# Optimization experiments

Hardware: AMD Instinct MI355X
Metric: run time of the kernel (lower is better)

Reference implementation:

```python
import jax, jax.numpy as jnp
import numpy as np

B, D, O = 512, 256, 128  # batch, input_dim, output_dim


def setup_inputs() -> dict:
    key = jax.random.key(0)
    k1, k2, k3, k4, k5, k6 = jax.random.split(key, 6)
    eyeD = jnp.eye(D, dtype=jnp.float32)
    # density-like inputs: diagonal offset keeps the trace denominator well-conditioned
    x_real = jax.random.normal(k1, (B, D, D), dtype=jnp.float32) + 2.0 * eyeD
    x_imag = jax.random.normal(k2, (B, D, D), dtype=jnp.float32)
    # weight = identity + small perturbation (module inits to [eye, zeros] stacked)
    w_r = eyeD + 0.02 * jax.random.normal(k3, (D, D), dtype=jnp.float32)
    w_i = 0.02 * jax.random.normal(k4, (D, D), dtype=jnp.float32)
    weight = jnp.stack([w_r, w_i], axis=-1)  # [D, D, 2]
    rand_w = jax.random.uniform(k5, (O,), dtype=jnp.float32)
    lam = jax.random.uniform(k6, (1,), dtype=jnp.float32)
    return {"x_real": x_real, "x_imag": x_imag, "weight": weight,
            "rand_w": rand_w, "lam": lam}


def reference(x_real, x_imag, weight, rand_w, lam):
    out_dim = rand_w.shape[0]
    U_r = weight[:, :, 0]  # [D, D]
    U_i = weight[:, :, 1]
    # evolution: (U_r + i U_i) X (U_r + i U_i)^H, batched over b
    R = jnp.einsum('ij,bjk->bik', U_r, x_real) - jnp.einsum('ij,bjk->bik', U_i, x_imag)
    I = jnp.einsum('ij,bjk->bik', U_i, x_real) + jnp.einsum('ij,bjk->bik', U_r, x_imag)
    out_r = jnp.einsum('bik,jk->bij', R, U_r) + jnp.einsum('bik,jk->bij', I, U_i)
    out_i = jnp.einsum('bik,jk->bij', I, U_r) - jnp.einsum('bik,jk->bij', R, U_i)
    # input_dim >= output_dim branch: top-left block, normalized by trace of real part
    sub_r = out_r[:, :out_dim, :out_dim]
    sub_i = out_i[:, :out_dim, :out_dim]
    tr = jnp.trace(sub_r, axis1=1, axis2=2)[:, None, None]  # [B,1,1]
    norm_r = sub_r / tr
    norm_i = sub_i / tr
    p = jax.nn.softmax(rand_w, axis=-1)
    s = jax.nn.sigmoid(lam[0])
    output_r = s * norm_r + (1.0 - s) * jnp.diag(p)
    output_i = s * norm_i
    return (output_r, output_i)
```

## Files before the change

kernel.cpp:

```cpp
#include <hip/hip_runtime.h>
#include <hip/hip_bf16.h>


typedef __attribute__((ext_vector_type(4))) float f32x4;
typedef __attribute__((ext_vector_type(8))) short bf16x8;

static __device__ __forceinline__ short f2bf(float f) {
    unsigned u = __float_as_uint(f);
    u += 0x7fffu + ((u >> 16) & 1u);
    return (short)(u >> 16);
}

static __device__ __forceinline__ unsigned cvtpk2(float lo, float hi) {
    union { __hip_bfloat162 h; unsigned u; } c;
    c.h = __float22bfloat162_rn(float2{lo, hi});
    return c.u;
}

static __device__ __forceinline__ uint2 cvt2(f32x4 v) {
    uint2 r;
    r.x = cvtpk2(v[0], v[1]);
    r.y = cvtpk2(v[2], v[3]);
    return r;
}

static __device__ __forceinline__ f32x4 mfma16(bf16x8 a, bf16x8 b, f32x4 c) {
    return __builtin_amdgcn_mfma_f32_16x16x32_bf16(a, b, c, 0, 0, 0);
}

__global__ void qprep_u(const float* __restrict__ wt,
                        short* __restrict__ Ur,  short* __restrict__ Ui,
                        short* __restrict__ Upr, short* __restrict__ Upi) {
    int idx = blockIdx.x * 256 + threadIdx.x;
    int j = idx >> 8, k = idx & 255;
    float2 v = ((const float2*)wt)[idx];
    short br = f2bf(v.x), bi = f2bf(v.y);
    Ur[idx] = br;
    Ui[idx] = bi;
    int g = j >> 4, s = k >> 5;
    int lanep = (j & 15) | (((k >> 3) & 3) << 4);
    int p = ((g * 8 + s) * 64 + lanep) * 8 + (k & 7);
    Upr[p] = br;
    Upi[p] = bi;
}

__global__ void qprep_ps(const float* __restrict__ rw, const float* __restrict__ lm,
                         float* __restrict__ pv, float* __restrict__ sv) {
    int t = threadIdx.x;
    float w0 = rw[t], w1 = rw[t + 64];
    float m = fmaxf(w0, w1);
    #pragma unroll
    for (int o = 32; o > 0; o >>= 1) m = fmaxf(m, __shfl_xor(m, o));
    float e0 = expf(w0 - m), e1 = expf(w1 - m);
    float ss = e0 + e1;
    #pragma unroll
    for (int o = 32; o > 0; o >>= 1) ss += __shfl_xor(ss, o);
    pv[t] = e0 / ss;
    pv[t + 64] = e1 / ss;
    if (t == 0) sv[0] = 1.f / (1.f + expf(-lm[0]));
}

__global__ void qprep_q(const float* __restrict__ wt,
                        short* __restrict__ Qrb, short* __restrict__ Qib) {
    int j = blockIdx.x;
    int k = threadIdx.x;
    float ar = 0.f, ai = 0.f;
    for (int i = 0; i < 128; ++i) {
        float2 uk = ((const float2*)wt)[i * 256 + k];
        float2 uj = ((const float2*)wt)[i * 256 + j];
        ar += uk.x * uj.x + uk.y * uj.y;
        ai += uk.x * uj.y - uk.y * uj.x;
    }
    Qrb[j * 256 + k] = f2bf(ar);
    Qib[j * 256 + k] = f2bf(ai);
}

#define SBASE(Q) (((Q) >> 1) * 64 + ((Q) & 1) * 32)
#define NBASE(Q) ((((Q) + 1) >> 1) * 64 + (((Q) + 1) & 1) * 32)

#define CONS(KS, TR) do {                                                       \
    const int ke = ((KS) + kk0) & 7;                                            \
    const int ko = ke * 64 + g16;                                               \
    bf16x8 axr = *(const bf16x8*)(xsp + aro + (ko ^ aswz));                     \
    bf16x8 axi = *(const bf16x8*)(xsp + 8192 + aro + (ko ^ aswz));              \
    bf16x8 bur = *(const bf16x8*)(smem + uob + (ko ^ uswz));                    \
    bf16x8 bui = *(const bf16x8*)(smem + 32768 + uob + (ko ^ uswz));            \
    bf16x8 axrn = axr ^ (short)0x8000;                                          \
    yR = mfma16(axr,  bur, yR);                                                 \
    yR = mfma16(axi,  bui, yR);                                                 \
    yI = mfma16(axi,  bur, yI);                                                 \
    yI = mfma16(axrn, bui, yI);                                                 \
    if ((TR) == 1) {                                                            \
        bf16x8 axin = axi ^ (short)0x8000;                                      \
        tr4 = mfma16(axr,  q0r, tr4);                                           \
        tr4 = mfma16(axin, q0i, tr4);                                           \
    }                                                                           \
    if ((TR) == 2) {                                                            \
        bf16x8 axin = axi ^ (short)0x8000;                                      \
        tr4 = mfma16(axr,  q1r, tr4);                                           \
        tr4 = mfma16(axin, q1i, tr4);                                           \
    }                                                                           \
} while (0)

#define PAIR(Q, LAST) do {                                                      \
    const char* xsp = smem + 81920 + ((Q) & 1) * 32768 + wj16k;                 \
           \
    f32x4 sa0, sa1, sa2, sa3;                                                   \
    if (!(LAST)) {                                                              \
        const int gr0 = (NBASE(Q) + sr0) * 256 + xl4;                           \
        const int gr1 = (NBASE(Q) + sr1) * 256 + xl4;                           \
        sa0 = *(const f32x4*)(xr + xgb + gr0);                                  \
        sa1 = *(const f32x4*)(xr + xgb + gr1);                                  \
        sa2 = *(const f32x4*)(xi + xgb + gr0);                                  \
        sa3 = *(const f32x4*)(xi + xgb + gr1);                                  \
    }                                                                           \
    __builtin_amdgcn_sched_barrier(0);                                          \
    CONS(0, 1);                                                                 \
    CONS(1, 2);                                                                 \
    CONS(2, 0);                                                                 \
    CONS(3, 0);                                                                 \
               \
    f32x4 sb0, sb1, sb2, sb3;                                                   \
    if (!(LAST)) {                                                              \
        char* wp = smem + 81920 + (((Q) + 1) & 1) * 32768;                      \
        *(uint2*)(wp + wr0o)        = cvt2(sa0);                                \
        *(uint2*)(wp + wr1o)        = cvt2(sa1);                                \
        *(uint2*)(wp + 8192 + wr0o) = cvt2(sa2);                                \
        *(uint2*)(wp + 8192 + wr1o) = cvt2(sa3);                                \
        const int qb = (NBASE(Q) + wj * 16 + c16) * 256 + kk0 * 32 + g8;        \
        q0r = *(const bf16x8*)(Qrb + qb);                                       \
        q0i = *(const bf16x8*)(Qib + qb);                                       \
        q1r = *(const bf16x8*)(Qrb + qb + 32);                                  \
        q1i = *(const bf16x8*)(Qib + qb + 32);                                  \
        const int gr0 = (NBASE(Q) + 16 + sr0) * 256 + xl4;                      \
        const int gr1 = (NBASE(Q) + 16 + sr1) * 256 + xl4;                      \
        sb0 = *(const f32x4*)(xr + xgb + gr0);                                  \
        sb1 = *(const f32x4*)(xr + xgb + gr1);                                  \
        sb2 = *(const f32x4*)(xi + xgb + gr0);                                  \
        sb3 = *(const f32x4*)(xi + xgb + gr1);                                  \
    }                                                                           \
    __builtin_amdgcn_sched_barrier(0);                                          \
    CONS(4, 0);                                                                 \
    CONS(5, 0);                                                                 \
    CONS(6, 0);                                                                 \
    CONS(7, 0);                                                                 \
    if (!(LAST)) {                                                              \
        char* wp = smem + 81920 + (((Q) + 1) & 1) * 32768 + 16384;              \
        *(uint2*)(wp + wr0o)        = cvt2(sb0);                                \
        *(uint2*)(wp + wr1o)        = cvt2(sb1);                                \
        *(uint2*)(wp + 8192 + wr0o) = cvt2(sb2);                                \
        *(uint2*)(wp + 8192 + wr1o) = cvt2(sb3);                                \
    }                                                                           \
                             \
    {                                                                           \
        const int yw = ((Q) & 1) ? ytw1 : ytw0;                                 \
        *(uint2*)(smem + 65536 + yw) = cvt2(yR);                                \
        *(uint2*)(smem + 73728 + yw) = cvt2(yI);                                \
    }                                                                           \
    yR = zero; yI = zero;                                                       \
    asm volatile("s_waitcnt lgkmcnt(0)" ::: "memory");                          \
    __builtin_amdgcn_sched_barrier(0);                                          \
    __builtin_amdgcn_s_barrier();                                               \
    __builtin_amdgcn_sched_barrier(0);                                          \
} while (0)

#define STAGEB_KS(JT, KS2) do {                                                 \
    const int s2 = (JT) * 2 + (KS2);                                            \
    bf16x8 aur0 = *(const bf16x8*)(Upr + ((wm * 2 + 0) * 8 + s2) * 512 + l8);   \
    bf16x8 aui0 = *(const bf16x8*)(Upi + ((wm * 2 + 0) * 8 + s2) * 512 + l8);   \
    bf16x8 aur1 = *(const bf16x8*)(Upr + ((wm * 2 + 1) * 8 + s2) * 512 + l8);   \
    bf16x8 aui1 = *(const bf16x8*)(Upi + ((wm * 2 + 1) * 8 + s2) * 512 + l8);   \
    bf16x8 auin0 = aui0 ^ (short)0x8000;                                        \
    bf16x8 auin1 = aui1 ^ (short)0x8000;                                        \
    {                                                                           \
        const int off = ybA + (((KS2) * 64 + g16) ^ ysA);                       \
        bf16x8 byr = *(const bf16x8*)(smem + 65536 + off);                      \
        bf16x8 byi = *(const bf16x8*)(smem + 73728 + off);                      \
        sR00 = mfma16(aur0,  byr, sR00); sR00 = mfma16(auin0, byi, sR00);       \
        sI00 = mfma16(aui0,  byr, sI00); sI00 = mfma16(aur0,  byi, sI00);       \
        sR10 = mfma16(aur1,  byr, sR10); sR10 = mfma16(auin1, byi, sR10);       \
        sI10 = mfma16(aui1,  byr, sI10); sI10 = mfma16(aur1,  byi, sI10);       \
    }                                                                           \
    {                                                                           \
        const int off = ybB + (((KS2) * 64 + g16) ^ ysB);                       \
        bf16x8 byr = *(const bf16x8*)(smem + 65536 + off);                      \
        bf16x8 byi = *(const bf16x8*)(smem + 73728 + off);                      \
        sR01 = mfma16(aur0,  byr, sR01); sR01 = mfma16(auin0, byi, sR01);       \
        sI01 = mfma16(aui0,  byr, sI01); sI01 = mfma16(aur0,  byi, sI01);       \
        sR11 = mfma16(aur1,  byr, sR11); sR11 = mfma16(auin1, byi, sR11);       \
        sI11 = mfma16(aui1,  byr, sI11); sI11 = mfma16(aur1,  byi, sI11);       \
    }                                                                           \
} while (0)

#define STAGEB_PASS(JT) do {                                                    \
    STAGEB_KS(JT, 0);                                                           \
    STAGEB_KS(JT, 1);                                                           \
    asm volatile("s_waitcnt lgkmcnt(0)" ::: "memory");                          \
    __builtin_amdgcn_sched_barrier(0);                                          \
    __builtin_amdgcn_s_barrier();         \
    __builtin_amdgcn_sched_barrier(0);                                          \
} while (0)

__global__ __launch_bounds__(512, 1) void qfused(
    const float* __restrict__ xr, const float* __restrict__ xi,
    const short* __restrict__ Urg, const short* __restrict__ Uig,
    const short* __restrict__ Upr, const short* __restrict__ Upi,
    const short* __restrict__ Qrb, const short* __restrict__ Qib,
    const float* __restrict__ pv, const float* __restrict__ sv,
    float* __restrict__ out)
{
    __shared__ __align__(16) char smem[147456];

    const int bx   = blockIdx.x;
    const int b    = bx >> 1;
    const int kh   = bx & 1;
    const int tid  = threadIdx.x;
    const int lane = tid & 63;
    const int w    = tid >> 6;
    const int c16  = lane & 15;
    const int g4   = lane >> 4;
    const int g8   = g4 * 8;
    const int g16  = g4 * 16;
    const int l8   = lane * 8;

    const int wj    = w >> 2;
    const int wk    = w & 3;
    const int kk0   = wk * 2;
    const int wj16k = wj * 16384;
    const int wm    = w >> 1;
    const int wn    = w & 1;

    const int sr0 = w * 2, sr1 = w * 2 + 1;
    const int xl4 = lane * 4;
    const int xgb = b << 16;
    const int wr0o = sr0 * 512 + ((((lane >> 1) << 4) ^ ((sr0 & 7) << 4))) + ((lane & 1) << 3);
    const int wr1o = sr1 * 512 + ((((lane >> 1) << 4) ^ ((sr1 & 7) << 4))) + ((lane & 1) << 3);

    const int aro  = c16 * 512;
    const int aswz = (c16 & 7) << 4;
    const int ukl  = wk * 16 + c16;
    const int uob  = ukl * 512;
    const int uswz = (ukl & 7) << 4;

    const int ytr  = ukl;
    const int ytk  = (ytr & 7) << 4;
    const int ytw0 = ytr * 128 + (((0 * 64) + wj * 32 + g8) ^ ytk);
    const int ytw1 = ytr * 128 + (((1 * 64) + wj * 32 + g8) ^ ytk);

    const int ybA = (wn * 32 + c16) * 128;
    const int ybB = (wn * 32 + 16 + c16) * 128;
    const int ysA = ((wn * 32 + c16) & 7) << 4;
    const int ysB = ((wn * 32 + 16 + c16) & 7) << 4;

    #pragma unroll
    for (int q = 0; q < 4; ++q) {
        int c    = tid + q * 512;
        int row  = c >> 5;
        int slot = c & 31;
        int ss   = slot ^ (row & 7);
        const short* sr = Urg + (size_t)(kh * 64 + row) * 256 + ss * 8;
        const short* si = Uig + (size_t)(kh * 64 + row) * 256 + ss * 8;
        *(bf16x8*)(smem + row * 512 + slot * 16)         = *(const bf16x8*)sr;
        *(bf16x8*)(smem + 32768 + row * 512 + slot * 16) = *(const bf16x8*)si;
    }

    f32x4 zero = {0.f, 0.f, 0.f, 0.f};
    f32x4 sR00 = zero, sR01 = zero, sR10 = zero, sR11 = zero;
    f32x4 sI00 = zero, sI01 = zero, sI10 = zero, sI11 = zero;
    f32x4 tr4 = zero;
    f32x4 yR = zero, yI = zero;
    bf16x8 q0r, q0i, q1r, q1i;

    {
        f32x4 a0 = *(const f32x4*)(xr + xgb + (0  + sr0) * 256 + xl4);
        f32x4 a1 = *(const f32x4*)(xr + xgb + (0  + sr1) * 256 + xl4);
        f32x4 a2 = *(const f32x4*)(xi + xgb + (0  + sr0) * 256 + xl4);
        f32x4 a3 = *(const f32x4*)(xi + xgb + (0  + sr1) * 256 + xl4);
        f32x4 b0 = *(const f32x4*)(xr + xgb + (16 + sr0) * 256 + xl4);
        f32x4 b1 = *(const f32x4*)(xr + xgb + (16 + sr1) * 256 + xl4);
        f32x4 b2 = *(const f32x4*)(xi + xgb + (16 + sr0) * 256 + xl4);
        f32x4 b3 = *(const f32x4*)(xi + xgb + (16 + sr1) * 256 + xl4);
        const int qb = (0 + wj * 16 + c16) * 256 + kk0 * 32 + g8;
        q0r = *(const bf16x8*)(Qrb + qb);
        q0i = *(const bf16x8*)(Qib + qb);
        q1r = *(const bf16x8*)(Qrb + qb + 32);
        q1i = *(const bf16x8*)(Qib + qb + 32);
        char* w0p = smem + 81920;
        char* w1p = smem + 81920 + 16384;
        *(uint2*)(w0p + wr0o)        = cvt2(a0);
        *(uint2*)(w0p + wr1o)        = cvt2(a1);
        *(uint2*)(w0p + 8192 + wr0o) = cvt2(a2);
        *(uint2*)(w0p + 8192 + wr1o) = cvt2(a3);
        *(uint2*)(w1p + wr0o)        = cvt2(b0);
        *(uint2*)(w1p + wr1o)        = cvt2(b1);
        *(uint2*)(w1p + 8192 + wr0o) = cvt2(b2);
        *(uint2*)(w1p + 8192 + wr1o) = cvt2(b3);
    }
    asm volatile("s_waitcnt lgkmcnt(0)" ::: "memory");
    __builtin_amdgcn_sched_barrier(0);
    __builtin_amdgcn_s_barrier();
    __builtin_amdgcn_sched_barrier(0);

    PAIR(0, 0);
    PAIR(1, 0);
    STAGEB_PASS(0);
    PAIR(2, 0);
    PAIR(3, 0);
    STAGEB_PASS(1);
    PAIR(4, 0);
    PAIR(5, 0);
    STAGEB_PASS(2);
    PAIR(6, 0);
    PAIR(7, 1);
    STAGEB_KS(3, 0);
    STAGEB_KS(3, 1);

    float loc = ((c16 >> 2) == g4) ? tr4[c16 & 3] : 0.f;
    #pragma unroll
    for (int o = 32; o > 0; o >>= 1) loc += __shfl_xor(loc, o);
    __syncthreads();
    float* red = (float*)(smem + 65536);
    if (lane == 0) red[w] = loc;
    __syncthreads();
    float tr = red[0] + red[1] + red[2] + red[3] +
               red[4] + red[5] + red[6] + red[7];

    float s     = sv[0];
    float inv   = s / tr;
    float onems = 1.f - s;
    float* outr = out + (size_t)b * 16384;
    float* outi = out + 8388608 + (size_t)b * 16384;

    #define EPI(SRV, SIV, MT, NT) do {                                          \
        int colc = kh * 64 + wn * 32 + (NT) * 16 + c16;                         \
        _Pragma("unroll")                                                       \
        for (int r = 0; r < 4; ++r) {                                           \
            int row = wm * 32 + (MT) * 16 + g4 * 4 + r;                         \
            float vr = SRV[r] * inv;                                            \
            if (row == colc) vr += onems * pv[row];                             \
            outr[row * 128 + colc] = vr;                                        \
            outi[row * 128 + colc] = SIV[r] * inv;                              \
        }                                                                       \
    } while (0)

    EPI(sR00, sI00, 0, 0);
    EPI(sR01, sI01, 0, 1);
    EPI(sR10, sI10, 1, 0);
    EPI(sR11, sI11, 1, 1);
    #undef EPI
}

extern "C" void kernel_launch(void* const* d_in, const int* in_sizes, int n_in,
                              void* d_out, int out_size, void* d_ws, size_t ws_size,
                              hipStream_t stream) {
    (void)in_sizes; (void)n_in; (void)out_size; (void)ws_size;
    const float* xr = (const float*)d_in[0];
    const float* xi = (const float*)d_in[1];
    const float* wt = (const float*)d_in[2];
    const float* rw = (const float*)d_in[3];
    const float* lm = (const float*)d_in[4];

    short* Ur  = (short*)d_ws;
    short* Ui  = (short*)((char*)d_ws + 65536);
    short* Upr = (short*)((char*)d_ws + 131072);
    short* Upi = (short*)((char*)d_ws + 196608);
    short* Qrb = (short*)((char*)d_ws + 262144);
    short* Qib = (short*)((char*)d_ws + 393216);
    float* pv  = (float*)((char*)d_ws + 524288);
    float* sv  = pv + 128;
    float* o   = (float*)d_out;

    qprep_u<<<dim3(128), dim3(256), 0, stream>>>(wt, Ur, Ui, Upr, Upi);
    qprep_ps<<<dim3(1), dim3(64), 0, stream>>>(rw, lm, pv, sv);
    qprep_q<<<dim3(256), dim3(256), 0, stream>>>(wt, Qrb, Qib);
    qfused<<<dim3(1024), dim3(512), 0, stream>>>(xr, xi, Ur, Ui, Upr, Upi,
                                                 Qrb, Qib, pv, sv, o);
}
```

Baseline: 171.2 us.

## Deepen global prefetch to two stages ahead and regroup block-to-batch mapping

```diff
diff --git a/kernel.cpp b/kernel.cpp
--- a/kernel.cpp
+++ b/kernel.cpp
@@ -75,8 +75,7 @@
     Qib[j * 256 + k] = f2bf(ai);
 }
 
-#define SBASE(Q) (((Q) >> 1) * 64 + ((Q) & 1) * 32)
-#define NBASE(Q) ((((Q) + 1) >> 1) * 64 + (((Q) + 1) & 1) * 32)
+#define PB(Q) ((Q) * 32)
 
 #define CONS(KS, TR) do {                                                       \
     const int ke = ((KS) + kk0) & 7;                                            \
@@ -102,56 +101,51 @@
     }                                                                           \
 } while (0)
 
-#define PAIR(Q, LAST) do {                                                      \
+#define PAIR(Q) do {                                                            \
     const char* xsp = smem + 81920 + ((Q) & 1) * 32768 + wj16k;                 \
-           \
-    f32x4 sa0, sa1, sa2, sa3;                                                   \
-    if (!(LAST)) {                                                              \
-        const int gr0 = (NBASE(Q) + sr0) * 256 + xl4;                           \
-        const int gr1 = (NBASE(Q) + sr1) * 256 + xl4;                           \
-        sa0 = *(const f32x4*)(xr + xgb + gr0);                                  \
-        sa1 = *(const f32x4*)(xr + xgb + gr1);                                  \
-        sa2 = *(const f32x4*)(xi + xgb + gr0);                                  \
-        sa3 = *(const f32x4*)(xi + xgb + gr1);                                  \
+    if ((Q) < 7) {                                                              \
+        char* wp0 = smem + 81920 + (((Q) + 1) & 1) * 32768;                     \
+        *(uint2*)(wp0 + wr0o)        = cvt2(pA0);                               \
+        *(uint2*)(wp0 + wr1o)        = cvt2(pA1);                               \
+        *(uint2*)(wp0 + 8192 + wr0o) = cvt2(pA2);                               \
+        *(uint2*)(wp0 + 8192 + wr1o) = cvt2(pA3);                               \
+        char* wp1 = wp0 + 16384;                                                \
+        *(uint2*)(wp1 + wr0o)        = cvt2(pB0);                               \
+        *(uint2*)(wp1 + wr1o)        = cvt2(pB1);                               \
+        *(uint2*)(wp1 + 8192 + wr0o) = cvt2(pB2);                               \
+        *(uint2*)(wp1 + 8192 + wr1o) = cvt2(pB3);                               \
+    }                                                                           \
+    if ((Q) < 6) {                                                              \
+        const int r0 = (PB((Q) + 2) + sr0) * 256 + xl4;                         \
+        const int r1 = (PB((Q) + 2) + sr1) * 256 + xl4;                         \
+        pA0 = *(const f32x4*)(xr + xgb + r0);                                   \
+        pA1 = *(const f32x4*)(xr + xgb + r1);                                   \
+        pA2 = *(const f32x4*)(xi + xgb + r0);                                   \
+        pA3 = *(const f32x4*)(xi + xgb + r1);                                   \
+        const int r2 = (PB((Q) + 2) + 16 + sr0) * 256 + xl4;                    \
+        const int r3 = (PB((Q) + 2) + 16 + sr1) * 256 + xl4;                    \
+        pB0 = *(const f32x4*)(xr + xgb + r2);                                   \
+        pB1 = *(const f32x4*)(xr + xgb + r3);                                   \
+        pB2 = *(const f32x4*)(xi + xgb + r2);                                   \
+        pB3 = *(const f32x4*)(xi + xgb + r3);                                   \
     }                                                                           \
     __builtin_amdgcn_sched_barrier(0);                                          \
     CONS(0, 1);                                                                 \
     CONS(1, 2);                                                                 \
     CONS(2, 0);                                                                 \
     CONS(3, 0);                                                                 \
-               \
-    f32x4 sb0, sb1, sb2, sb3;                                                   \
-    if (!(LAST)) {                                                              \
-        char* wp = smem + 81920 + (((Q) + 1) & 1) * 32768;                      \
-        *(uint2*)(wp + wr0o)        = cvt2(sa0);                                \
-        *(uint2*)(wp + wr1o)        = cvt2(sa1);                                \
-        *(uint2*)(wp + 8192 + wr0o) = cvt2(sa2);                                \
-        *(uint2*)(wp + 8192 + wr1o) = cvt2(sa3);                                \
-        const int qb = (NBASE(Q) + wj * 16 + c16) * 256 + kk0 * 32 + g8;        \
+    if ((Q) < 7) {        \
+        const int qb = (PB((Q) + 1) + wj * 16 + c16) * 256 + kk0 * 32 + g8;     \
         q0r = *(const bf16x8*)(Qrb + qb);                                       \
         q0i = *(const bf16x8*)(Qib + qb);                                       \
         q1r = *(const bf16x8*)(Qrb + qb + 32);                                  \
         q1i = *(const bf16x8*)(Qib + qb + 32);                                  \
-        const int gr0 = (NBASE(Q) + 16 + sr0) * 256 + xl4;                      \
-        const int gr1 = (NBASE(Q) + 16 + sr1) * 256 + xl4;                      \
-        sb0 = *(const f32x4*)(xr + xgb + gr0);                                  \
-        sb1 = *(const f32x4*)(xr + xgb + gr1);                                  \
-        sb2 = *(const f32x4*)(xi + xgb + gr0);                                  \
-        sb3 = *(const f32x4*)(xi + xgb + gr1);                                  \
     }                                                                           \
     __builtin_amdgcn_sched_barrier(0);                                          \
     CONS(4, 0);                                                                 \
     CONS(5, 0);                                                                 \
     CONS(6, 0);                                                                 \
     CONS(7, 0);                                                                 \
-    if (!(LAST)) {                                                              \
-        char* wp = smem + 81920 + (((Q) + 1) & 1) * 32768 + 16384;              \
-        *(uint2*)(wp + wr0o)        = cvt2(sb0);                                \
-        *(uint2*)(wp + wr1o)        = cvt2(sb1);                                \
-        *(uint2*)(wp + 8192 + wr0o) = cvt2(sb2);                                \
-        *(uint2*)(wp + 8192 + wr1o) = cvt2(sb3);                                \
-    }                                                                           \
-                             \
     {                                                                           \
         const int yw = ((Q) & 1) ? ytw1 : ytw0;                                 \
         *(uint2*)(smem + 65536 + yw) = cvt2(yR);                                \
@@ -212,8 +206,8 @@
     __shared__ __align__(16) char smem[147456];
 
     const int bx   = blockIdx.x;
-    const int b    = bx >> 1;
-    const int kh   = bx & 1;
+    const int b    = ((bx >> 4) << 3) | (bx & 7);
+    const int kh   = (bx >> 3) & 1;
     const int tid  = threadIdx.x;
     const int lane = tid & 63;
     const int w    = tid >> 6;
@@ -244,8 +238,8 @@
 
     const int ytr  = ukl;
     const int ytk  = (ytr & 7) << 4;
-    const int ytw0 = ytr * 128 + (((0 * 64) + wj * 32 + g8) ^ ytk);
-    const int ytw1 = ytr * 128 + (((1 * 64) + wj * 32 + g8) ^ ytk);
+    const int ytw0 = ytr * 128 + ((wj * 32 + g8) ^ ytk);
+    const int ytw1 = ytr * 128 + ((64 + wj * 32 + g8) ^ ytk);
 
     const int ybA = (wn * 32 + c16) * 128;
     const int ybB = (wn * 32 + 16 + c16) * 128;
@@ -270,17 +264,35 @@
     f32x4 tr4 = zero;
     f32x4 yR = zero, yI = zero;
     bf16x8 q0r, q0i, q1r, q1i;
+    f32x4 pA0, pA1, pA2, pA3;
+    f32x4 pB0, pB1, pB2, pB3;
 
     {
-        f32x4 a0 = *(const f32x4*)(xr + xgb + (0  + sr0) * 256 + xl4);
-        f32x4 a1 = *(const f32x4*)(xr + xgb + (0  + sr1) * 256 + xl4);
-        f32x4 a2 = *(const f32x4*)(xi + xgb + (0  + sr0) * 256 + xl4);
-        f32x4 a3 = *(const f32x4*)(xi + xgb + (0  + sr1) * 256 + xl4);
-        f32x4 b0 = *(const f32x4*)(xr + xgb + (16 + sr0) * 256 + xl4);
-        f32x4 b1 = *(const f32x4*)(xr + xgb + (16 + sr1) * 256 + xl4);
-        f32x4 b2 = *(const f32x4*)(xi + xgb + (16 + sr0) * 256 + xl4);
-        f32x4 b3 = *(const f32x4*)(xi + xgb + (16 + sr1) * 256 + xl4);
-        const int qb = (0 + wj * 16 + c16) * 256 + kk0 * 32 + g8;
+        const int r0 = (PB(0) + sr0) * 256 + xl4;
+        const int r1 = (PB(0) + sr1) * 256 + xl4;
+        const int r2 = (PB(0) + 16 + sr0) * 256 + xl4;
+        const int r3 = (PB(0) + 16 + sr1) * 256 + xl4;
+        f32x4 a0 = *(const f32x4*)(xr + xgb + r0);
+        f32x4 a1 = *(const f32x4*)(xr + xgb + r1);
+        f32x4 a2 = *(const f32x4*)(xi + xgb + r0);
+        f32x4 a3 = *(const f32x4*)(xi + xgb + r1);
+        f32x4 b0 = *(const f32x4*)(xr + xgb + r2);
+        f32x4 b1 = *(const f32x4*)(xr + xgb + r3);
+        f32x4 b2 = *(const f32x4*)(xi + xgb + r2);
+        f32x4 b3 = *(const f32x4*)(xi + xgb + r3);
+        const int r4 = (PB(1) + sr0) * 256 + xl4;
+        const int r5 = (PB(1) + sr1) * 256 + xl4;
+        const int r6 = (PB(1) + 16 + sr0) * 256 + xl4;
+        const int r7 = (PB(1) + 16 + sr1) * 256 + xl4;
+        pA0 = *(const f32x4*)(xr + xgb + r4);
+        pA1 = *(const f32x4*)(xr + xgb + r5);
+        pA2 = *(const f32x4*)(xi + xgb + r4);
+        pA3 = *(const f32x4*)(xi + xgb + r5);
+        pB0 = *(const f32x4*)(xr + xgb + r6);
+        pB1 = *(const f32x4*)(xr + xgb + r7);
+        pB2 = *(const f32x4*)(xi + xgb + r6);
+        pB3 = *(const f32x4*)(xi + xgb + r7);
+        const int qb = (PB(0) + wj * 16 + c16) * 256 + kk0 * 32 + g8;
         q0r = *(const bf16x8*)(Qrb + qb);
         q0i = *(const bf16x8*)(Qib + qb);
         q1r = *(const bf16x8*)(Qrb + qb + 32);
@@ -301,17 +313,17 @@
     __builtin_amdgcn_s_barrier();
     __builtin_amdgcn_sched_barrier(0);
 
-    PAIR(0, 0);
-    PAIR(1, 0);
+    PAIR(0);
+    PAIR(1);
     STAGEB_PASS(0);
-    PAIR(2, 0);
-    PAIR(3, 0);
+    PAIR(2);
+    PAIR(3);
     STAGEB_PASS(1);
-    PAIR(4, 0);
-    PAIR(5, 0);
+    PAIR(4);
+    PAIR(5);
     STAGEB_PASS(2);
-    PAIR(6, 0);
-    PAIR(7, 1);
+    PAIR(6);
+    PAIR(7);
     STAGEB_KS(3, 0);
     STAGEB_KS(3, 1);
 
```

Result: faster. 163.7 us (-4.4%).
